# Kernel optimization log

Hardware: AMD Instinct MI355X
Metric: run time of the kernel (lower is better)

Reference implementation:

```python
import jax, jax.numpy as jnp
import numpy as np

D_MODEL = 1024
NHEAD = 16
D_HEAD = D_MODEL // NHEAD
D_FF = 2 * D_MODEL
EPS = 1e-5


def setup_inputs() -> dict:
    key = jax.random.key(0)
    ks = jax.random.split(key, 12)
    s = 1.0 / np.sqrt(D_MODEL)
    x = jax.random.normal(ks[0], (4, 1024, D_MODEL), dtype=jnp.float32)
    # per-head projections stacked: [H, d_model, d_head] (x @ W layout)
    wq = jax.random.normal(ks[1], (NHEAD, D_MODEL, D_HEAD), dtype=jnp.float32) * s
    bq = jnp.zeros((NHEAD, D_HEAD), dtype=jnp.float32)
    wk = jax.random.normal(ks[2], (NHEAD, D_MODEL, D_HEAD), dtype=jnp.float32) * s
    bk = jnp.zeros((NHEAD, D_HEAD), dtype=jnp.float32)
    wv = jax.random.normal(ks[3], (NHEAD, D_MODEL, D_HEAD), dtype=jnp.float32) * s
    bv = jnp.zeros((NHEAD, D_HEAD), dtype=jnp.float32)
    wo_w = jax.random.normal(ks[4], (D_MODEL, D_MODEL), dtype=jnp.float32) * s
    wo_b = jnp.zeros((D_MODEL,), dtype=jnp.float32)
    ff1_w = jax.random.normal(ks[5], (D_MODEL, D_FF), dtype=jnp.float32) * s
    ff1_b = jnp.zeros((D_FF,), dtype=jnp.float32)
    ff2_w = jax.random.normal(ks[6], (D_FF, D_MODEL), dtype=jnp.float32) * (1.0 / np.sqrt(D_FF))
    ff2_b = jnp.zeros((D_MODEL,), dtype=jnp.float32)
    g1 = jnp.ones((D_MODEL,), dtype=jnp.float32)
    b1 = jnp.zeros((D_MODEL,), dtype=jnp.float32)
    g2 = jnp.ones((D_MODEL,), dtype=jnp.float32)
    b2 = jnp.zeros((D_MODEL,), dtype=jnp.float32)
    return dict(x=x, wq=wq, bq=bq, wk=wk, bk=bk, wv=wv, bv=bv,
                wo_w=wo_w, wo_b=wo_b, g1=g1, b1=b1,
                ff1_w=ff1_w, ff1_b=ff1_b, ff2_w=ff2_w, ff2_b=ff2_b,
                g2=g2, b2=b2)


def manual_layernorm(x, gamma, beta):
    # faithful to source: (x - mean) / (std + eps), std unbiased=False
    mean = jnp.mean(x, axis=-1, keepdims=True)
    std = jnp.sqrt(jnp.mean((x - mean) ** 2, axis=-1, keepdims=True))
    return gamma * (x - mean) / (std + EPS) + beta


def reference(x, wq, bq, wk, bk, wv, bv, wo_w, wo_b, g1, b1,
              ff1_w, ff1_b, ff2_w, ff2_b, g2, b2):
    B, S, D = x.shape
    # per-head projections, vectorized over heads: [B,H,S,d_head]
    q = jnp.einsum('bsd,hdk->bhsk', x, wq) + bq[None, :, None, :]
    k = jnp.einsum('bsd,hdk->bhsk', x, wk) + bk[None, :, None, :]
    v = jnp.einsum('bsd,hdk->bhsk', x, wv) + bv[None, :, None, :]
    scores = jnp.einsum('bhsk,bhtk->bhst', q, k) / jnp.sqrt(jnp.float32(D_HEAD))
    weights = jax.nn.softmax(scores, axis=-1)
    attn = jnp.einsum('bhst,bhtk->bhsk', weights, v)
    # concat heads back to [B,S,D]
    concat = jnp.transpose(attn, (0, 2, 1, 3)).reshape(B, S, D)
    proj = concat @ wo_w + wo_b
    h = manual_layernorm(x + proj, g1, b1)
    ff = jax.nn.relu(h @ ff1_w + ff1_b) @ ff2_w + ff2_b
    return manual_layernorm(h + ff, g2, b2)
```

## Files before the change

kernel.cpp:

```cpp
#include <hip/hip_runtime.h>
#include <hip/hip_bf16.h>

typedef __attribute__((ext_vector_type(8))) short bf16x8;
typedef __attribute__((ext_vector_type(4))) float f32x4;
using bf16 = __hip_bfloat16;

#define NTOK 4096
#define EPS_LN 1e-5f
#define QSCL 0.1803368801111244f

enum { EPI_F32 = 0, EPI_QKV = 1, EPI_RELU_BF16 = 2 };

#define VM8 asm volatile("s_waitcnt vmcnt(8)" ::: "memory")
#define VM0 asm volatile("s_waitcnt vmcnt(0)" ::: "memory")
#define LGKM0 asm volatile("s_waitcnt lgkmcnt(0)" ::: "memory")
#define SCHED0 __builtin_amdgcn_sched_barrier(0)
#define NOVM
#define DSRO(dst, ad, off) \
  asm volatile("ds_read_b128 %0, %1 offset:" #off : "=v"(dst) : "v"(ad))

__device__ inline void gload_lds16(const void* g, void* l) {
  __builtin_amdgcn_global_load_lds(
      (const __attribute__((address_space(1))) char*)g,
      (__attribute__((address_space(3))) char*)l, 16, 0, 0);
}

__device__ inline unsigned ldsoff(const void* p) {
  return (unsigned)(size_t)(const __attribute__((address_space(3))) char*)p;
}

__device__ inline unsigned short f2bfu(float x) {
  bf16 h = __float2bfloat16(x);
  return __builtin_bit_cast(unsigned short, h);
}
__device__ inline bf16 to_bf16(float v) { return __float2bfloat16(v); }
__device__ inline bf16 to_bf16(bf16 v) { return v; }


__global__ __launch_bounds__(256) void cvt_bf16_kernel(const float* __restrict__ src,
                                                       bf16* __restrict__ dst, int n4) {
  int i = blockIdx.x * 256 + threadIdx.x;
  if (i >= n4) return;
  float4 v = ((const float4*)src)[i];
  ushort4 o;
  o.x = f2bfu(v.x); o.y = f2bfu(v.y); o.z = f2bfu(v.z); o.w = f2bfu(v.w);
  ((ushort4*)dst)[i] = o;
}

template <typename ST>
__global__ __launch_bounds__(256) void transpose_cvt(const ST* __restrict__ src,
                                                     bf16* __restrict__ dst, int R, int C) {
  __shared__ bf16 tile[32][33];
  int o = blockIdx.z;
  int r0 = blockIdx.y * 32, c0 = blockIdx.x * 32;
  int tx = threadIdx.x & 31, ty = threadIdx.x >> 5;
  const ST* s = src + (size_t)o * R * C;
  bf16* d = dst + (size_t)o * R * C;
#pragma unroll
  for (int i = 0; i < 32; i += 8)
    tile[ty + i][tx] = to_bf16(s[(size_t)(r0 + ty + i) * C + (c0 + tx)]);
  __syncthreads();
#pragma unroll
  for (int i = 0; i < 32; i += 8)
    d[(size_t)(c0 + ty + i) * R + (r0 + tx)] = tile[tx][ty + i];
}

__global__ __launch_bounds__(256) void pack_bias_kernel(const float* __restrict__ bq,
                                                        const float* __restrict__ bk,
                                                        const float* __restrict__ bv,
                                                        float* __restrict__ out) {
  int i = blockIdx.x * 256 + threadIdx.x;
  if (i >= 3072) return;
  out[i] = (i < 1024) ? bq[i] : (i < 2048 ? bk[i - 1024] : bv[i - 2048]);
}


#define STG(KOFF, DD) { _Pragma("unroll") for (int q = 0; q < 4; ++q) { \
    gload_lds16(gA0 + (KOFF) + (size_t)(q * 32) * lda2, \
                sAb + (DD) * 16384 + q * 4096 + w * 1024); \
    gload_lds16(gB0 + (KOFF) + (size_t)(q * 32) * ldb2, \
                sBb + (DD) * 16384 + q * 4096 + w * 1024); } }

#define TILE(OFFLIT, STG_, VMS) { \
  _Pragma("unroll") for (int i = 0; i < 4; ++i) { \
    DSRO(a[i][0], adA[i][0], OFFLIT); \
    DSRO(a[i][1], adA[i][1], OFFLIT); \
  } \
  _Pragma("unroll") for (int j = 0; j < 4; ++j) { \
    DSRO(b[j][0], adB[j][0], OFFLIT); \
    DSRO(b[j][1], adB[j][1], OFFLIT); \
  } \
  LGKM0; SCHED0; \
  __builtin_amdgcn_s_barrier(); \
  STG_; \
  __builtin_amdgcn_s_setprio(1); \
  _Pragma("unroll") for (int i = 0; i < 4; ++i) \
  _Pragma("unroll") for (int j = 0; j < 4; ++j) \
  _Pragma("unroll") for (int kk = 0; kk < 2; ++kk) \
    acc[i][j] = __builtin_amdgcn_mfma_f32_16x16x32_bf16( \
        a[i][kk], b[j][kk], acc[i][j], 0, 0, 0); \
  __builtin_amdgcn_s_setprio(0); \
  VMS; \
  __builtin_amdgcn_s_barrier(); }

__global__ __launch_bounds__(256, 2) void gemm128(
    const bf16* __restrict__ A, int lda,
    const bf16* __restrict__ Bt, int ldb,
    int M, int N, int K,
    int nbm, int nbn,
    const float* __restrict__ bias,
    float* __restrict__ Cf, bf16* __restrict__ Cb,
    bf16* __restrict__ Qd, bf16* __restrict__ Kd, bf16* __restrict__ Vd,
    int mode) {
  __shared__ bf16 sA[2][128][64];
  __shared__ bf16 sB[2][128][64];
  const int nwg = nbm * nbn;
  const int orig = blockIdx.x;
  const int wgid = (orig % 8) * (nwg / 8) + orig / 8;
  const int bm = wgid / nbn, bn = wgid % nbn;
  const int tid = threadIdx.x;
  const int w = tid >> 6, lane = tid & 63;
  const int wm = w >> 1, wn = w & 1;
  const int ri = lane & 15, kg = lane >> 4;
  const bf16* Ab = A + (size_t)bm * 128 * lda;
  const bf16* Bb = Bt + (size_t)bn * 128 * ldb;
  const int NT = K / 64;
  const size_t lda2 = (size_t)lda * 2, ldb2 = (size_t)ldb * 2;
  char* sAb = (char*)&sA[0][0][0];
  char* sBb = (char*)&sB[0][0][0];

  unsigned adA[4][2], adB[4][2];
  const unsigned sA0 = ldsoff(sAb), sB0 = ldsoff(sBb);
#pragma unroll
  for (int i = 0; i < 4; ++i) {
    int row = wm * 64 + i * 16 + ri;
    unsigned swz = (unsigned)((row & 7) << 4);
    adA[i][0] = sA0 + row * 128 + ((kg * 16) ^ swz);
    adA[i][1] = sA0 + row * 128 + ((64 + kg * 16) ^ swz);
  }
#pragma unroll
  for (int j = 0; j < 4; ++j) {
    int row = wn * 64 + j * 16 + ri;
    unsigned swz = (unsigned)((row & 7) << 4);
    adB[j][0] = sB0 + row * 128 + ((kg * 16) ^ swz);
    adB[j][1] = sB0 + row * 128 + ((64 + kg * 16) ^ swz);
  }

  const int r0 = tid >> 3;
  const int cb0 = ((tid & 7) * 16) ^ ((r0 & 7) << 4);
  const char* gA0 = (const char*)Ab + (size_t)r0 * lda2 + cb0;
  const char* gB0 = (const char*)Bb + (size_t)r0 * ldb2 + cb0;

  f32x4 acc[4][4] = {};
  bf16x8 a[4][2], b[4][2];

  STG(0, 0) STG(128, 1)
  VM8;
  __builtin_amdgcn_s_barrier();

  const int niter = NT / 2 - 1;
  for (int it = 0; it < niter; ++it) {
    TILE(0,     STG(256, 0), VM8)
    TILE(16384, STG(384, 1), VM8)
    gA0 += 256; gB0 += 256;
  }
  TILE(0,     , VM0)
  TILE(16384, , NOVM)

  const int colbase = bn * 128 + wn * 64 + ri;
  float bv4[4];
#pragma unroll
  for (int nf = 0; nf < 4; ++nf)
    bv4[nf] = bias ? bias[colbase + nf * 16] : 0.f;

  if (mode == EPI_QKV) {
    int col0 = bn * 128 + wn * 64;
    int which = col0 >> 10, hh = (col0 >> 6) & 15;
    bf16* dst = (which == 0) ? Qd : (which == 1) ? Kd : Vd;
    float scl = (which == 0) ? QSCL : 1.0f;
#pragma unroll
    for (int mf = 0; mf < 4; ++mf)
#pragma unroll
      for (int r = 0; r < 4; ++r) {
        int row = bm * 128 + wm * 64 + mf * 16 + kg * 4 + r;
        int b2 = row >> 10, s = row & 1023;
        bf16* o = dst + (((size_t)(b2 * 16 + hh)) * 1024 + s) * 64;
#pragma unroll
        for (int nf = 0; nf < 4; ++nf)
          o[nf * 16 + ri] = __float2bfloat16((acc[mf][nf][r] + bv4[nf]) * scl);
      }
  } else if (mode == EPI_F32) {
#pragma unroll
    for (int mf = 0; mf < 4; ++mf)
#pragma unroll
      for (int r = 0; r < 4; ++r) {
        int row = bm * 128 + wm * 64 + mf * 16 + kg * 4 + r;
        float* o = Cf + (size_t)row * N + colbase;
#pragma unroll
        for (int nf = 0; nf < 4; ++nf) o[nf * 16] = acc[mf][nf][r] + bv4[nf];
      }
  } else {
#pragma unroll
    for (int mf = 0; mf < 4; ++mf)
#pragma unroll
      for (int r = 0; r < 4; ++r) {
        int row = bm * 128 + wm * 64 + mf * 16 + kg * 4 + r;
        bf16* o = Cb + (size_t)row * N + colbase;
#pragma unroll
        for (int nf = 0; nf < 4; ++nf) {
          float v = acc[mf][nf][r] + bv4[nf];
          o[nf * 16] = __float2bfloat16(v > 0.f ? v : 0.f);
        }
      }
  }
}

__global__ __launch_bounds__(256, 4) void attn_kernel(
    const bf16* __restrict__ Qb, const bf16* __restrict__ Kb,
    const bf16* __restrict__ Vs, bf16* __restrict__ Ob) {
  __shared__ bf16 KV[2][2][64][64];
  __shared__ bf16 Ps[4][16][64];
  const int orig = blockIdx.x;
  const int blk = (orig & 7) * 128 + (orig >> 3);
  const int bh = blk >> 4, qt = blk & 15;
  const int bb = bh >> 4, hh = bh & 15;
  const int tid = threadIdx.x, w = tid >> 6, lane = tid & 63;
  const int ri = lane & 15, kg = lane >> 4, r8 = lane >> 3;
  const int cb = ((lane & 7) * 16) ^ ((r8 & 7) << 4);
  const unsigned rsw = (unsigned)((ri & 7) << 4);
  const bf16* qp = Qb + (size_t)bh * 65536;
  const bf16* kp = Kb + (size_t)bh * 65536;
  const bf16* vp = Vs + (size_t)bh * 65536;
  const int q0 = qt * 64 + w * 16;
  const int c0 = w * 2, c1 = c0 + 1;

  unsigned offk0 = (unsigned)((kg * 16) ^ (int)rsw);
  unsigned offk1 = (unsigned)((64 + kg * 16) ^ (int)rsw);
  unsigned adF[4][2];
  const unsigned kv0 = ldsoff(&KV[0][0][0][0]);
#pragma unroll
  for (int n = 0; n < 4; ++n) {
    unsigned row = (unsigned)((n * 16 + ri) * 128);
    adF[n][0] = kv0 + row + offk0;
    adF[n][1] = kv0 + row + offk1;
  }
  const unsigned ps0 = ldsoff(&Ps[0][0][0]) + (unsigned)(w * 2048 + ri * 128);
  unsigned adPr[2] = {ps0 + offk0, ps0 + offk1};
  char* pwb = (char*)&Ps[0][0][0] + w * 2048 + ri * 128;

  bf16x8 qf[2];
  qf[0] = *(const bf16x8*)(qp + (size_t)(q0 + ri) * 64 + kg * 8);
  qf[1] = *(const bf16x8*)(qp + (size_t)(q0 + ri) * 64 + 32 + kg * 8);

  f32x4 oacc[4] = {};
  float mrun = -1e30f, lrun = 0.f;

#define ASTAGE(T, D) { \
    gload_lds16((const char*)(kp + (size_t)((T) * 64 + c0 * 8 + r8) * 64) + cb, \
                (char*)KV + (D) * 16384 + c0 * 1024); \
    gload_lds16((const char*)(kp + (size_t)((T) * 64 + c1 * 8 + r8) * 64) + cb, \
                (char*)KV + (D) * 16384 + c1 * 1024); \
    gload_lds16((const char*)(vp + (size_t)(c0 * 8 + r8) * 1024 + (T) * 64) + cb, \
                (char*)KV + (D) * 16384 + 8192 + c0 * 1024); \
    gload_lds16((const char*)(vp + (size_t)(c1 * 8 + r8) * 1024 + (T) * 64) + cb, \
                (char*)KV + (D) * 16384 + 8192 + c1 * 1024); }

  ASTAGE(0, 0);
  VM0;
  __syncthreads();

  for (int t = 0; t < 16; ++t) {
    const int cur = t & 1;
    if (t < 15) ASTAGE(t + 1, cur ^ 1);
    const unsigned bo = (unsigned)(cur * 16384);

    bf16x8 kf[2][4];
#pragma unroll
    for (int n = 0; n < 4; ++n) {
      DSRO(kf[0][n], adF[n][0] + bo, 0);
      DSRO(kf[1][n], adF[n][1] + bo, 0);
    }
    LGKM0; SCHED0;
    f32x4 sac[4] = {};
#pragma unroll
    for (int n = 0; n < 4; ++n) {
      sac[n] = __builtin_amdgcn_mfma_f32_16x16x32_bf16(kf[0][n], qf[0], sac[n], 0, 0, 0);
      sac[n] = __builtin_amdgcn_mfma_f32_16x16x32_bf16(kf[1][n], qf[1], sac[n], 0, 0, 0);
    }

    float mx[4];
#pragma unroll
    for (int n = 0; n < 4; ++n)
      mx[n] = fmaxf(fmaxf(sac[n][0], sac[n][1]), fmaxf(sac[n][2], sac[n][3]));
    float mt = fmaxf(fmaxf(mx[0], mx[1]), fmaxf(mx[2], mx[3]));
    mt = fmaxf(mt, __shfl_xor(mt, 16));
    mt = fmaxf(mt, __shfl_xor(mt, 32));
    if (!__all(mt - mrun <= 8.f)) {
      float mnew = fmaxf(mrun, mt);
      float corr = exp2f(mrun - mnew);
      mrun = mnew;
      lrun *= corr;
      float cr[4];
#pragma unroll
      for (int r = 0; r < 4; ++r) cr[r] = __shfl(corr, kg * 4 + r);
#pragma unroll
      for (int n = 0; n < 4; ++n) {
        oacc[n][0] *= cr[0]; oacc[n][1] *= cr[1];
        oacc[n][2] *= cr[2]; oacc[n][3] *= cr[3];
      }
    }
    float p[4][4];
    float su[4];
#pragma unroll
    for (int n = 0; n < 4; ++n) {
      p[n][0] = exp2f(sac[n][0] - mrun); p[n][1] = exp2f(sac[n][1] - mrun);
      p[n][2] = exp2f(sac[n][2] - mrun); p[n][3] = exp2f(sac[n][3] - mrun);
      su[n] = (p[n][0] + p[n][1]) + (p[n][2] + p[n][3]);
    }
    float sum = (su[0] + su[1]) + (su[2] + su[3]);
    sum += __shfl_xor(sum, 16);
    sum += __shfl_xor(sum, 32);
    lrun += sum;
#pragma unroll
    for (int n = 0; n < 4; ++n) {
      ushort4 pk;
      pk.x = f2bfu(p[n][0]); pk.y = f2bfu(p[n][1]);
      pk.z = f2bfu(p[n][2]); pk.w = f2bfu(p[n][3]);
      *(ushort4*)(pwb + (((n * 32 + kg * 8)) ^ (int)rsw)) = pk;
    }
    LGKM0;

    bf16x8 pf[2], vf[2][4];
    DSRO(pf[0], adPr[0], 0);
    DSRO(pf[1], adPr[1], 0);
#pragma unroll
    for (int n = 0; n < 4; ++n) {
      DSRO(vf[0][n], adF[n][0] + bo, 8192);
      DSRO(vf[1][n], adF[n][1] + bo, 8192);
    }
    LGKM0; SCHED0;
#pragma unroll
    for (int n = 0; n < 4; ++n) {
      oacc[n] = __builtin_amdgcn_mfma_f32_16x16x32_bf16(pf[0], vf[0][n], oacc[n], 0, 0, 0);
      oacc[n] = __builtin_amdgcn_mfma_f32_16x16x32_bf16(pf[1], vf[1][n], oacc[n], 0, 0, 0);
    }
    if (t < 15) {
      VM0;
      __syncthreads();
    }
  }

  float inv = 1.f / lrun;
  float ivr[4];
#pragma unroll
  for (int r = 0; r < 4; ++r) ivr[r] = __shfl(inv, kg * 4 + r);
#pragma unroll
  for (int r = 0; r < 4; ++r) {
    int s = q0 + kg * 4 + r;
    size_t base = ((size_t)(bb * 1024 + s)) * 1024 + hh * 64;
#pragma unroll
    for (int n = 0; n < 4; ++n)
      Ob[base + n * 16 + ri] = __float2bfloat16(oacc[n][r] * ivr[r]);
  }
#undef ASTAGE
}

__global__ __launch_bounds__(256) void ln_kernel(
    const float* __restrict__ a, const float* __restrict__ b,
    const float* __restrict__ gamma, const float* __restrict__ beta,
    float* __restrict__ out_f32, bf16* __restrict__ out_bf16) {
  int row = blockIdx.x;
  int tid = threadIdx.x;
  float4 av = ((const float4*)(a + (size_t)row * 1024))[tid];
  float4 bv = ((const float4*)(b + (size_t)row * 1024))[tid];
  float4 z;
  z.x = av.x + bv.x; z.y = av.y + bv.y; z.z = av.z + bv.z; z.w = av.w + bv.w;
  float s = z.x + z.y + z.z + z.w;
  float ss = z.x * z.x + z.y * z.y + z.z * z.z + z.w * z.w;
#pragma unroll
  for (int o = 32; o >= 1; o >>= 1) { s += __shfl_xor(s, o); ss += __shfl_xor(ss, o); }
  __shared__ float red[8];
  int wid = tid >> 6;
  if ((tid & 63) == 0) { red[wid] = s; red[4 + wid] = ss; }
  __syncthreads();
  s = red[0] + red[1] + red[2] + red[3];
  ss = red[4] + red[5] + red[6] + red[7];
  float mean = s * (1.f / 1024.f);
  float var = ss * (1.f / 1024.f) - mean * mean;
  var = var > 0.f ? var : 0.f;
  float inv = 1.f / (sqrtf(var) + EPS_LN);
  float4 g = ((const float4*)gamma)[tid];
  float4 be = ((const float4*)beta)[tid];
  float4 y;
  y.x = (z.x - mean) * inv * g.x + be.x;
  y.y = (z.y - mean) * inv * g.y + be.y;
  y.z = (z.z - mean) * inv * g.z + be.z;
  y.w = (z.w - mean) * inv * g.w + be.w;
  ((float4*)(out_f32 + (size_t)row * 1024))[tid] = y;
  if (out_bf16) {
    ushort4 o;
    o.x = f2bfu(y.x); o.y = f2bfu(y.y); o.z = f2bfu(y.z); o.w = f2bfu(y.w);
    ((ushort4*)(out_bf16 + (size_t)row * 1024))[tid] = o;
  }
}

extern "C" void kernel_launch(void* const* d_in, const int* in_sizes, int n_in,
                              void* d_out, int out_size, void* d_ws, size_t ws_size,
                              hipStream_t stream) {
  const float* x = (const float*)d_in[0];
  const float* wq = (const float*)d_in[1];
  const float* bq = (const float*)d_in[2];
  const float* wk = (const float*)d_in[3];
  const float* bk = (const float*)d_in[4];
  const float* wv = (const float*)d_in[5];
  const float* bv = (const float*)d_in[6];
  const float* wo_w = (const float*)d_in[7];
  const float* wo_b = (const float*)d_in[8];
  const float* g1 = (const float*)d_in[9];
  const float* b1 = (const float*)d_in[10];
  const float* ff1w = (const float*)d_in[11];
  const float* ff1b = (const float*)d_in[12];
  const float* ff2w = (const float*)d_in[13];
  const float* ff2b = (const float*)d_in[14];
  const float* g2 = (const float*)d_in[15];
  const float* b2 = (const float*)d_in[16];

  char* ws = (char*)d_ws;
  size_t off = 0;
  auto alloc = [&](size_t bytes) {
    char* p = ws + off;
    off += (bytes + 255) & ~(size_t)255;
    return p;
  };
  bf16* xb = (bf16*)alloc((size_t)NTOK * 1024 * 2);
  bf16* wqkvt = (bf16*)alloc((size_t)3072 * 1024 * 2);
  bf16* wot = (bf16*)alloc((size_t)1024 * 1024 * 2);
  bf16* ff1t = (bf16*)alloc((size_t)2048 * 1024 * 2);
  bf16* ff2t = (bf16*)alloc((size_t)1024 * 2048 * 2);
  float* qkvbias = (float*)alloc(3072 * 4);
  bf16* qbuf = (bf16*)alloc((size_t)64 * 1024 * 64 * 2);
  bf16* kbuf = (bf16*)alloc((size_t)64 * 1024 * 64 * 2);
  bf16* vbuf = (bf16*)alloc((size_t)64 * 1024 * 64 * 2);
  bf16* vtb = (bf16*)alloc((size_t)64 * 64 * 1024 * 2);
  bf16* attnb = (bf16*)alloc((size_t)NTOK * 1024 * 2);
  float* proj = (float*)alloc((size_t)NTOK * 1024 * 4);
  bf16* hb = (bf16*)alloc((size_t)NTOK * 1024 * 2);
  bf16* ff1o = qbuf;
  float* hbuf = (float*)d_out;

  cvt_bf16_kernel<<<(NTOK * 1024 / 4 + 255) / 256, 256, 0, stream>>>(x, xb, NTOK * 1024 / 4);
  transpose_cvt<float><<<dim3(2, 32, 16), 256, 0, stream>>>(wq, wqkvt, 1024, 64);
  transpose_cvt<float><<<dim3(2, 32, 16), 256, 0, stream>>>(wk, wqkvt + 1024 * 1024, 1024, 64);
  transpose_cvt<float><<<dim3(2, 32, 16), 256, 0, stream>>>(wv, wqkvt + 2 * 1024 * 1024, 1024, 64);
  transpose_cvt<float><<<dim3(32, 32, 1), 256, 0, stream>>>(wo_w, wot, 1024, 1024);
  transpose_cvt<float><<<dim3(64, 32, 1), 256, 0, stream>>>(ff1w, ff1t, 1024, 2048);
  transpose_cvt<float><<<dim3(32, 64, 1), 256, 0, stream>>>(ff2w, ff2t, 2048, 1024);
  pack_bias_kernel<<<12, 256, 0, stream>>>(bq, bk, bv, qkvbias);

  gemm128<<<768, 256, 0, stream>>>(xb, 1024, wqkvt, 1024, 4096, 3072, 1024,
                                   32, 24, qkvbias,
                                   nullptr, nullptr, qbuf, kbuf, vbuf, EPI_QKV);
  transpose_cvt<bf16><<<dim3(2, 32, 64), 256, 0, stream>>>(vbuf, vtb, 1024, 64);
  attn_kernel<<<dim3(1024), 256, 0, stream>>>(qbuf, kbuf, vtb, attnb);
  gemm128<<<256, 256, 0, stream>>>(attnb, 1024, wot, 1024, 4096, 1024, 1024,
                                   32, 8, wo_b,
                                   proj, nullptr, nullptr, nullptr, nullptr, EPI_F32);
  ln_kernel<<<4096, 256, 0, stream>>>(x, proj, g1, b1, hbuf, hb);
  gemm128<<<512, 256, 0, stream>>>(hb, 1024, ff1t, 1024, 4096, 2048, 1024,
                                   32, 16, ff1b,
                                   nullptr, ff1o, nullptr, nullptr, nullptr, EPI_RELU_BF16);
  gemm128<<<256, 256, 0, stream>>>(ff1o, 2048, ff2t, 2048, 4096, 1024, 2048,
                                   32, 8, ff2b,
                                   proj, nullptr, nullptr, nullptr, nullptr, EPI_F32);
  ln_kernel<<<4096, 256, 0, stream>>>(hbuf, proj, g2, b2, (float*)d_out, nullptr);
}
```

Baseline: 176.8 us.

## Process two query fragments per wave in attention to reuse K/V tiles

Each attention block now handles 128 queries instead of 64, with every wave owning two 16-row query fragments that share the same K/V tiles staged in LDS. This halves the grid to 512 blocks and halves global K/V loads per query. It also amortizes barrier and staging overhead across more work. In exchange it adds register pressure (the launch-bounds occupancy hint drops from 4 to 3), serializes the two fragments through a single P staging buffer, and may underfill the GPU's compute units with fewer blocks.

```diff
diff --git a/kernel.cpp b/kernel.cpp
--- a/kernel.cpp
+++ b/kernel.cpp
@@ -215,14 +215,14 @@
   }
 }
 
-__global__ __launch_bounds__(256, 4) void attn_kernel(
+__global__ __launch_bounds__(256, 3) void attn_kernel(
     const bf16* __restrict__ Qb, const bf16* __restrict__ Kb,
     const bf16* __restrict__ Vs, bf16* __restrict__ Ob) {
   __shared__ bf16 KV[2][2][64][64];
   __shared__ bf16 Ps[4][16][64];
   const int orig = blockIdx.x;
-  const int blk = (orig & 7) * 128 + (orig >> 3);
-  const int bh = blk >> 4, qt = blk & 15;
+  const int blk = (orig & 7) * 64 + (orig >> 3);
+  const int bh = blk >> 3, qb = blk & 7;
   const int bb = bh >> 4, hh = bh & 15;
   const int tid = threadIdx.x, w = tid >> 6, lane = tid & 63;
   const int ri = lane & 15, kg = lane >> 4, r8 = lane >> 3;
@@ -231,7 +231,7 @@
   const bf16* qp = Qb + (size_t)bh * 65536;
   const bf16* kp = Kb + (size_t)bh * 65536;
   const bf16* vp = Vs + (size_t)bh * 65536;
-  const int q0 = qt * 64 + w * 16;
+  const int q0 = qb * 128 + w * 32;
   const int c0 = w * 2, c1 = c0 + 1;
 
   unsigned offk0 = (unsigned)((kg * 16) ^ (int)rsw);
@@ -248,12 +248,15 @@
   unsigned adPr[2] = {ps0 + offk0, ps0 + offk1};
   char* pwb = (char*)&Ps[0][0][0] + w * 2048 + ri * 128;
 
-  bf16x8 qf[2];
-  qf[0] = *(const bf16x8*)(qp + (size_t)(q0 + ri) * 64 + kg * 8);
-  qf[1] = *(const bf16x8*)(qp + (size_t)(q0 + ri) * 64 + 32 + kg * 8);
-
-  f32x4 oacc[4] = {};
-  float mrun = -1e30f, lrun = 0.f;
+  bf16x8 qf[2][2];
+#pragma unroll
+  for (int f = 0; f < 2; ++f) {
+    qf[f][0] = *(const bf16x8*)(qp + (size_t)(q0 + f * 16 + ri) * 64 + kg * 8);
+    qf[f][1] = *(const bf16x8*)(qp + (size_t)(q0 + f * 16 + ri) * 64 + 32 + kg * 8);
+  }
+
+  f32x4 oacc[2][4] = {};
+  float mrun[2] = {-1e30f, -1e30f}, lrun[2] = {0.f, 0.f};
 
 #define ASTAGE(T, D) { \
     gload_lds16((const char*)(kp + (size_t)((T) * 64 + c0 * 8 + r8) * 64) + cb, \
@@ -281,68 +284,73 @@
       DSRO(kf[1][n], adF[n][1] + bo, 0);
     }
     LGKM0; SCHED0;
-    f32x4 sac[4] = {};
-#pragma unroll
-    for (int n = 0; n < 4; ++n) {
-      sac[n] = __builtin_amdgcn_mfma_f32_16x16x32_bf16(kf[0][n], qf[0], sac[n], 0, 0, 0);
-      sac[n] = __builtin_amdgcn_mfma_f32_16x16x32_bf16(kf[1][n], qf[1], sac[n], 0, 0, 0);
-    }
-
-    float mx[4];
-#pragma unroll
-    for (int n = 0; n < 4; ++n)
-      mx[n] = fmaxf(fmaxf(sac[n][0], sac[n][1]), fmaxf(sac[n][2], sac[n][3]));
-    float mt = fmaxf(fmaxf(mx[0], mx[1]), fmaxf(mx[2], mx[3]));
-    mt = fmaxf(mt, __shfl_xor(mt, 16));
-    mt = fmaxf(mt, __shfl_xor(mt, 32));
-    if (!__all(mt - mrun <= 8.f)) {
-      float mnew = fmaxf(mrun, mt);
-      float corr = exp2f(mrun - mnew);
-      mrun = mnew;
-      lrun *= corr;
-      float cr[4];
-#pragma unroll
-      for (int r = 0; r < 4; ++r) cr[r] = __shfl(corr, kg * 4 + r);
+    f32x4 sac[2][4] = {};
+#pragma unroll
+    for (int f = 0; f < 2; ++f)
 #pragma unroll
       for (int n = 0; n < 4; ++n) {
-        oacc[n][0] *= cr[0]; oacc[n][1] *= cr[1];
-        oacc[n][2] *= cr[2]; oacc[n][3] *= cr[3];
-      }
-    }
-    float p[4][4];
-    float su[4];
-#pragma unroll
-    for (int n = 0; n < 4; ++n) {
-      p[n][0] = exp2f(sac[n][0] - mrun); p[n][1] = exp2f(sac[n][1] - mrun);
-      p[n][2] = exp2f(sac[n][2] - mrun); p[n][3] = exp2f(sac[n][3] - mrun);
-      su[n] = (p[n][0] + p[n][1]) + (p[n][2] + p[n][3]);
-    }
-    float sum = (su[0] + su[1]) + (su[2] + su[3]);
-    sum += __shfl_xor(sum, 16);
-    sum += __shfl_xor(sum, 32);
-    lrun += sum;
-#pragma unroll
-    for (int n = 0; n < 4; ++n) {
-      ushort4 pk;
-      pk.x = f2bfu(p[n][0]); pk.y = f2bfu(p[n][1]);
-      pk.z = f2bfu(p[n][2]); pk.w = f2bfu(p[n][3]);
-      *(ushort4*)(pwb + (((n * 32 + kg * 8)) ^ (int)rsw)) = pk;
-    }
-    LGKM0;
-
-    bf16x8 pf[2], vf[2][4];
-    DSRO(pf[0], adPr[0], 0);
-    DSRO(pf[1], adPr[1], 0);
-#pragma unroll
-    for (int n = 0; n < 4; ++n) {
-      DSRO(vf[0][n], adF[n][0] + bo, 8192);
-      DSRO(vf[1][n], adF[n][1] + bo, 8192);
-    }
-    LGKM0; SCHED0;
-#pragma unroll
-    for (int n = 0; n < 4; ++n) {
-      oacc[n] = __builtin_amdgcn_mfma_f32_16x16x32_bf16(pf[0], vf[0][n], oacc[n], 0, 0, 0);
-      oacc[n] = __builtin_amdgcn_mfma_f32_16x16x32_bf16(pf[1], vf[1][n], oacc[n], 0, 0, 0);
+        sac[f][n] = __builtin_amdgcn_mfma_f32_16x16x32_bf16(kf[0][n], qf[f][0], sac[f][n], 0, 0, 0);
+        sac[f][n] = __builtin_amdgcn_mfma_f32_16x16x32_bf16(kf[1][n], qf[f][1], sac[f][n], 0, 0, 0);
+      }
+
+#pragma unroll
+    for (int f = 0; f < 2; ++f) {
+      float mx[4];
+#pragma unroll
+      for (int n = 0; n < 4; ++n)
+        mx[n] = fmaxf(fmaxf(sac[f][n][0], sac[f][n][1]), fmaxf(sac[f][n][2], sac[f][n][3]));
+      float mt = fmaxf(fmaxf(mx[0], mx[1]), fmaxf(mx[2], mx[3]));
+      mt = fmaxf(mt, __shfl_xor(mt, 16));
+      mt = fmaxf(mt, __shfl_xor(mt, 32));
+      if (!__all(mt - mrun[f] <= 8.f)) {
+        float mnew = fmaxf(mrun[f], mt);
+        float corr = exp2f(mrun[f] - mnew);
+        mrun[f] = mnew;
+        lrun[f] *= corr;
+        float cr[4];
+#pragma unroll
+        for (int r = 0; r < 4; ++r) cr[r] = __shfl(corr, kg * 4 + r);
+#pragma unroll
+        for (int n = 0; n < 4; ++n) {
+          oacc[f][n][0] *= cr[0]; oacc[f][n][1] *= cr[1];
+          oacc[f][n][2] *= cr[2]; oacc[f][n][3] *= cr[3];
+        }
+      }
+      float p[4][4];
+      float su[4];
+#pragma unroll
+      for (int n = 0; n < 4; ++n) {
+        p[n][0] = exp2f(sac[f][n][0] - mrun[f]); p[n][1] = exp2f(sac[f][n][1] - mrun[f]);
+        p[n][2] = exp2f(sac[f][n][2] - mrun[f]); p[n][3] = exp2f(sac[f][n][3] - mrun[f]);
+        su[n] = (p[n][0] + p[n][1]) + (p[n][2] + p[n][3]);
+      }
+      float sum = (su[0] + su[1]) + (su[2] + su[3]);
+      sum += __shfl_xor(sum, 16);
+      sum += __shfl_xor(sum, 32);
+      lrun[f] += sum;
+#pragma unroll
+      for (int n = 0; n < 4; ++n) {
+        ushort4 pk;
+        pk.x = f2bfu(p[n][0]); pk.y = f2bfu(p[n][1]);
+        pk.z = f2bfu(p[n][2]); pk.w = f2bfu(p[n][3]);
+        *(ushort4*)(pwb + (((n * 32 + kg * 8)) ^ (int)rsw)) = pk;
+      }
+      LGKM0;
+
+      bf16x8 pf[2], vf[2][4];
+      DSRO(pf[0], adPr[0], 0);
+      DSRO(pf[1], adPr[1], 0);
+#pragma unroll
+      for (int n = 0; n < 4; ++n) {
+        DSRO(vf[0][n], adF[n][0] + bo, 8192);
+        DSRO(vf[1][n], adF[n][1] + bo, 8192);
+      }
+      LGKM0; SCHED0;
+#pragma unroll
+      for (int n = 0; n < 4; ++n) {
+        oacc[f][n] = __builtin_amdgcn_mfma_f32_16x16x32_bf16(pf[0], vf[0][n], oacc[f][n], 0, 0, 0);
+        oacc[f][n] = __builtin_amdgcn_mfma_f32_16x16x32_bf16(pf[1], vf[1][n], oacc[f][n], 0, 0, 0);
+      }
     }
     if (t < 15) {
       VM0;
@@ -350,17 +358,20 @@
     }
   }
 
-  float inv = 1.f / lrun;
-  float ivr[4];
-#pragma unroll
-  for (int r = 0; r < 4; ++r) ivr[r] = __shfl(inv, kg * 4 + r);
-#pragma unroll
-  for (int r = 0; r < 4; ++r) {
-    int s = q0 + kg * 4 + r;
-    size_t base = ((size_t)(bb * 1024 + s)) * 1024 + hh * 64;
-#pragma unroll
-    for (int n = 0; n < 4; ++n)
-      Ob[base + n * 16 + ri] = __float2bfloat16(oacc[n][r] * ivr[r]);
+#pragma unroll
+  for (int f = 0; f < 2; ++f) {
+    float inv = 1.f / lrun[f];
+    float ivr[4];
+#pragma unroll
+    for (int r = 0; r < 4; ++r) ivr[r] = __shfl(inv, kg * 4 + r);
+#pragma unroll
+    for (int r = 0; r < 4; ++r) {
+      int s = q0 + f * 16 + kg * 4 + r;
+      size_t base = ((size_t)(bb * 1024 + s)) * 1024 + hh * 64;
+#pragma unroll
+      for (int n = 0; n < 4; ++n)
+        Ob[base + n * 16 + ri] = __float2bfloat16(oacc[f][n][r] * ivr[r]);
+    }
   }
 #undef ASTAGE
 }
@@ -461,7 +472,7 @@
                                    32, 24, qkvbias,
                                    nullptr, nullptr, qbuf, kbuf, vbuf, EPI_QKV);
   transpose_cvt<bf16><<<dim3(2, 32, 64), 256, 0, stream>>>(vbuf, vtb, 1024, 64);
-  attn_kernel<<<dim3(1024), 256, 0, stream>>>(qbuf, kbuf, vtb, attnb);
+  attn_kernel<<<dim3(512), 256, 0, stream>>>(qbuf, kbuf, vtb, attnb);
   gemm128<<<256, 256, 0, stream>>>(attnb, 1024, wot, 1024, 4096, 1024, 1024,
                                    32, 8, wo_b,
                                    proj, nullptr, nullptr, nullptr, nullptr, EPI_F32);
```

New measurement: 178.6 us. No clear change (+1.0%).
